# Performance work log

Measured on AMD Instinct MI355X. Metric: run time of the kernel, lower is better.

## Reference

```python
import jax, jax.numpy as jnp
import numpy as np

N = 50000   # nodes
E = 800000  # edges
F = 128     # feat_dim
LN_EPS = 1e-5


def setup_inputs() -> dict:
    key = jax.random.key(0)
    ks = jax.random.split(key, 16)

    def lin(k, fan_in, shape):
        # roughly kaiming-uniform-like scale; exact init is irrelevant for correctness
        return jax.random.normal(k, shape, jnp.float32) * (1.0 / np.sqrt(fan_in))

    inp = {
        "x": jax.random.normal(ks[0], (N, F), jnp.float32),
        "pos": jax.random.normal(ks[1], (N, 3), jnp.float32),
        "edge_index": jax.random.randint(ks[2], (2, E), 0, N, jnp.int64),
        # edge_mlp: Linear(2F+1 -> F), SiLU, Linear(F -> F)
        "ew1": lin(ks[3], 2 * F + 1, (2 * F + 1, F)),
        "eb1": jnp.zeros((F,), jnp.float32),
        "ew2": lin(ks[4], F, (F, F)),
        "eb2": jnp.zeros((F,), jnp.float32),
        # node_mlp: Linear(F -> F), SiLU, Linear(F -> F)
        "nw1": lin(ks[5], F, (F, F)),
        "nb1": jnp.zeros((F,), jnp.float32),
        "nw2": lin(ks[6], F, (F, F)),
        "nb2": jnp.zeros((F,), jnp.float32),
        # coord_mlp: Linear(F -> 1), Tanh
        "cw": lin(ks[7], F, (F, 1)),
        "cb": jnp.zeros((1,), jnp.float32),
        # LayerNorm(F)
        "gamma": jnp.ones((F,), jnp.float32),
        "beta": jnp.zeros((F,), jnp.float32),
    }
    return inp


def reference(x, pos, edge_index, ew1, eb1, ew2, eb2, nw1, nb1, nw2, nb2, cw, cb, gamma, beta):
    row, col = edge_index[0], edge_index[1]

    diff = pos[row] - pos[col]                              # [E, 3]
    dist2 = jnp.sum(diff * diff, axis=1, keepdims=True)     # [E, 1]
    edge_feat = jnp.concatenate([x[row], x[col], dist2], axis=1)  # [E, 2F+1]

    # edge MLP (dropout p=0 -> identity in eval)
    msg = jax.nn.silu(edge_feat @ ew1 + eb1) @ ew2 + eb2    # [E, F]

    # scatter-add messages to source nodes
    agg = jax.ops.segment_sum(msg, row, num_segments=N)     # [N, F]

    # node MLP + residual + LayerNorm
    upd = jax.nn.silu(agg @ nw1 + nb1) @ nw2 + nb2          # [N, F]
    pre = x + upd
    mean = jnp.mean(pre, axis=-1, keepdims=True)
    var = jnp.mean(jnp.square(pre - mean), axis=-1, keepdims=True)
    x_out = gamma * (pre - mean) * jax.lax.rsqrt(var + LN_EPS) + beta

    # coordinate update
    scale = jnp.tanh(msg @ cw + cb)                         # [E, 1]
    delta = jax.ops.segment_sum(scale * diff, row, num_segments=N)  # [N, 3]
    pos_out = pos + delta
    return (x_out, pos_out)
```

## Files before the change

### kernel.cpp

```cpp
#include <hip/hip_runtime.h>
#include <math.h>

#define NN 50000
#define EE 800000
#define FF 128

constexpr float LN_EPS = 1e-5f;
constexpr int NC = (NN + 255) / 256;

typedef float  f32x4  __attribute__((ext_vector_type(4)));
typedef short  s16x8  __attribute__((ext_vector_type(8)));

__device__ __forceinline__ float silu_f(float v) {
    return v / (1.f + __expf(-v));
}

__device__ __forceinline__ unsigned short f2bf(float f) {
    union { float f; unsigned u; } cv; cv.f = f;
    unsigned u = cv.u;
    u += 0x7fffu + ((u >> 16) & 1u);
    return (unsigned short)(u >> 16);
}

__device__ __forceinline__ float bf2f(unsigned short u) {
    union { unsigned u; float f; } cv; cv.u = ((unsigned)u) << 16;
    return cv.f;
}

__global__ __launch_bounds__(256) void convert_x_kernel(
    const float* __restrict__ x, unsigned short* __restrict__ xb)
{
    int i = (blockIdx.x * 256 + threadIdx.x) * 8;
    float4 a = *(const float4*)&x[i];
    float4 b = *(const float4*)&x[i + 4];
    s16x8 o;
    o[0] = (short)f2bf(a.x); o[1] = (short)f2bf(a.y);
    o[2] = (short)f2bf(a.z); o[3] = (short)f2bf(a.w);
    o[4] = (short)f2bf(b.x); o[5] = (short)f2bf(b.y);
    o[6] = (short)f2bf(b.z); o[7] = (short)f2bf(b.w);
    *(s16x8*)&xb[i] = o;
}

__global__ __launch_bounds__(256) void transpose_w_kernel(
    const float* __restrict__ ew1, const float* __restrict__ ew2,
    const float* __restrict__ nw1, const float* __restrict__ nw2,
    unsigned short* __restrict__ ew1T, unsigned short* __restrict__ ew2T,
    unsigned short* __restrict__ nw1T, unsigned short* __restrict__ nw2T)
{
    int o = blockIdx.x * 256 + threadIdx.x;
    if (o < 32768) {
        int n = o >> 8, k = o & 255;
        ew1T[o] = f2bf(ew1[k * FF + n]);
    } else if (o < 49152) {
        int o2 = o - 32768; int n = o2 >> 7, k = o2 & 127;
        ew2T[o2] = f2bf(ew2[k * FF + n]);
    } else if (o < 65536) {
        int o2 = o - 49152; int n = o2 >> 7, k = o2 & 127;
        nw1T[o2] = f2bf(nw1[k * FF + n]);
    } else {
        int o2 = o - 65536; int n = o2 >> 7, k = o2 & 127;
        nw2T[o2] = f2bf(nw2[k * FF + n]);
    }
}

__global__ __launch_bounds__(256) void hist_kernel(
    const int* __restrict__ ei, int* __restrict__ cnt)
{
    int e = blockIdx.x * 256 + threadIdx.x;
    if (e < EE) atomicAdd(&cnt[ei[e]], 1);
}

__global__ __launch_bounds__(256) void chunk_sum_kernel(
    const int* __restrict__ cnt, int* __restrict__ chunkSum)
{
    __shared__ int s[256];
    int t = threadIdx.x;
    int idx = blockIdx.x * 256 + t;
    s[t] = (idx < NN) ? cnt[idx] : 0;
    __syncthreads();
    for (int off = 128; off > 0; off >>= 1) {
        if (t < off) s[t] += s[t + off];
        __syncthreads();
    }
    if (t == 0) chunkSum[blockIdx.x] = s[0];
}

__global__ __launch_bounds__(256) void scan_chunks_kernel(
    const int* __restrict__ chunkSum, int* __restrict__ chunkOff)
{
    __shared__ int s[256];
    int t = threadIdx.x;
    int v = (t < NC) ? chunkSum[t] : 0;
    s[t] = v;
    __syncthreads();
    for (int off = 1; off < 256; off <<= 1) {
        int u = (t >= off) ? s[t - off] : 0;
        __syncthreads();
        s[t] += u;
        __syncthreads();
    }
    if (t < NC) chunkOff[t] = s[t] - v;
}

__global__ __launch_bounds__(256) void scan_kernel(
    const int* __restrict__ cnt, const int* __restrict__ chunkOff,
    int* __restrict__ offs, int* __restrict__ rowStart)
{
    __shared__ int s[256];
    int t = threadIdx.x;
    int idx = blockIdx.x * 256 + t;
    int v = (idx < NN) ? cnt[idx] : 0;
    s[t] = v;
    __syncthreads();
    for (int off = 1; off < 256; off <<= 1) {
        int u = (t >= off) ? s[t - off] : 0;
        __syncthreads();
        s[t] += u;
        __syncthreads();
    }
    if (idx < NN) {
        int st = chunkOff[blockIdx.x] + s[t] - v;
        offs[idx] = st;
        rowStart[idx] = st;
    }
}

__global__ __launch_bounds__(256) void scatter_idx_kernel(
    const int* __restrict__ ei, int* __restrict__ offs,
    int* __restrict__ sRow, int* __restrict__ sCol)
{
    int e = blockIdx.x * 256 + threadIdx.x;
    if (e < EE) {
        int r = ei[e], c = ei[EE + e];
        int p = atomicAdd(&offs[r], 1);
        sRow[p] = r;
        sCol[p] = c;
    }
}

constexpr int EPB   = 64;
constexpr int NTILE = EE / EPB;
constexpr int XAS   = 264;
constexpr int H1S   = 136;

__global__ __launch_bounds__(512, 4) void edgeA_kernel(
    const unsigned short* __restrict__ xb, const float* __restrict__ pos,
    const int* __restrict__ sRow, const int* __restrict__ sCol,
    const unsigned short* __restrict__ ew1T, const float* __restrict__ ew1,
    const float* __restrict__ eb1,
    const unsigned short* __restrict__ ew2T, const float* __restrict__ eb2,
    const float* __restrict__ cw,  const float* __restrict__ cb,
    unsigned short* __restrict__ msgb, float* __restrict__ sSg)
{
    __shared__ float dist2S[EPB];
    __shared__ float sPart[8][EPB];
    __shared__ __align__(16) unsigned short xa  [EPB * XAS];
    __shared__ __align__(16) unsigned short h1  [EPB * H1S];
    __shared__ __align__(16) unsigned short msgL[EPB * H1S];

    const int t   = threadIdx.x;
    const int w   = t >> 6;
    const int l   = t & 63;
    const int l15 = l & 15;
    const int q8  = l >> 4;
    const int n   = w * 16 + l15;

    s16x8 B1[8], B2[4];
    #pragma unroll
    for (int ko = 0; ko < 8; ++ko)
        B1[ko] = *(const s16x8*)(ew1T + (size_t)n * 256 + ko * 32 + q8 * 8);
    #pragma unroll
    for (int ko = 0; ko < 4; ++ko)
        B2[ko] = *(const s16x8*)(ew2T + (size_t)n * 128 + ko * 32 + q8 * 8);
    const float w256 = ew1[256 * FF + n];
    const float b1   = eb1[n];
    const float b2   = eb2[n];
    const float cwc  = cw[n];
    const float cb0  = cb[0];

    const int q   = t & 31;
    const int eB  = t >> 5;
    const int ksel = (q & 15) * 8;
    const int* idxBase = (q < 16) ? sRow : sCol;

    int   nidx[4];
    s16x8 ag[4];
    {
        int e0 = blockIdx.x * EPB;
        #pragma unroll
        for (int i = 0; i < 4; ++i) nidx[i] = idxBase[e0 + eB + 16 * i];
        #pragma unroll
        for (int i = 0; i < 4; ++i) ag[i] = *(const s16x8*)(xb + (size_t)nidx[i] * FF + ksel);
    }

    for (int tile = blockIdx.x; tile < NTILE; tile += gridDim.x) {
        const int e0 = tile * EPB;

        #pragma unroll
        for (int i = 0; i < 4; ++i)
            *(s16x8*)(xa + (eB + 16 * i) * XAS + q * 8) = ag[i];
        if (t < EPB) {
            int r = sRow[e0 + t];
            int c = sCol[e0 + t];
            float dx = pos[r*3+0] - pos[c*3+0];
            float dy = pos[r*3+1] - pos[c*3+1];
            float dz = pos[r*3+2] - pos[c*3+2];
            dist2S[t] = dx*dx + dy*dy + dz*dz;
        }
        __syncthreads();

        {
            int tn  = tile + gridDim.x;
            int e0n = (tn < NTILE) ? tn * EPB : 0;
            #pragma unroll
            for (int i = 0; i < 4; ++i) nidx[i] = idxBase[e0n + eB + 16 * i];
            #pragma unroll
            for (int i = 0; i < 4; ++i) ag[i] = *(const s16x8*)(xb + (size_t)nidx[i] * FF + ksel);
        }

        f32x4 acc[4] = {};
        #pragma unroll
        for (int mt = 0; mt < 4; ++mt) {
            const unsigned short* ar = xa + (mt * 16 + l15) * XAS + q8 * 8;
            #pragma unroll
            for (int ko = 0; ko < 8; ++ko) {
                s16x8 a = *(const s16x8*)(ar + ko * 32);
                acc[mt] = __builtin_amdgcn_mfma_f32_16x16x32_bf16(a, B1[ko], acc[mt], 0, 0, 0);
            }
        }

        #pragma unroll
        for (int mt = 0; mt < 4; ++mt) {
            #pragma unroll
            for (int r = 0; r < 4; ++r) {
                int e = mt * 16 + q8 * 4 + r;
                float v = acc[mt][r] + dist2S[e] * w256 + b1;
                h1[e * H1S + n] = f2bf(silu_f(v));
            }
        }
        __syncthreads();

        f32x4 acc2[4] = {};
        #pragma unroll
        for (int mt = 0; mt < 4; ++mt) {
            const unsigned short* hr = h1 + (mt * 16 + l15) * H1S + q8 * 8;
            #pragma unroll
            for (int ko = 0; ko < 4; ++ko) {
                s16x8 a = *(const s16x8*)(hr + ko * 32);
                acc2[mt] = __builtin_amdgcn_mfma_f32_16x16x32_bf16(a, B2[ko], acc2[mt], 0, 0, 0);
            }
        }

        #pragma unroll
        for (int mt = 0; mt < 4; ++mt) {
            #pragma unroll
            for (int r = 0; r < 4; ++r) {
                float m = acc2[mt][r] + b2;
                float p = m * cwc;
                p += __shfl_xor(p, 1);
                p += __shfl_xor(p, 2);
                p += __shfl_xor(p, 4);
                p += __shfl_xor(p, 8);
                int e = mt * 16 + q8 * 4 + r;
                if (l15 == 0) sPart[w][e] = p;
                msgL[e * H1S + n] = f2bf(m);
            }
        }
        __syncthreads();

        if (t < EPB) {
            float p = 0.f;
            #pragma unroll
            for (int ww = 0; ww < 8; ++ww) p += sPart[ww][t];
            sSg[e0 + t] = tanhf(p + cb0);
        }

        #pragma unroll
        for (int i = 0; i < 2; ++i) {
            int idx = i * 512 + t;
            int e   = idx >> 4;
            int c   = idx & 15;
            *(s16x8*)&msgb[(size_t)(e0 + e) * FF + c * 8] =
                *(const s16x8*)&msgL[e * H1S + c * 8];
        }
    }
}

constexpr int NPB = 16;
constexpr int ABS = 136;

__global__ __launch_bounds__(512) void nodeB_kernel(
    const float* __restrict__ x, const float* __restrict__ pos,
    const unsigned short* __restrict__ msgb, const float* __restrict__ sSg,
    const int* __restrict__ sCol, const int* __restrict__ rowStart,
    const unsigned short* __restrict__ nw1T, const float* __restrict__ nb1,
    const unsigned short* __restrict__ nw2T, const float* __restrict__ nb2,
    const float* __restrict__ gamma, const float* __restrict__ beta,
    float* __restrict__ xout, float* __restrict__ posout)
{
    __shared__ __align__(16) unsigned short aB [NPB * ABS];
    __shared__ __align__(16) unsigned short h1B[NPB * ABS];
    __shared__ float sRedS[8][NPB];
    __shared__ float sRedQ[8][NPB];

    const int t   = threadIdx.x;
    const int w   = t >> 6;
    const int l   = t & 63;
    const int l15 = l & 15;
    const int q8  = l >> 4;
    const int n0  = blockIdx.x * NPB;
    const int n   = w * 16 + l15;

    #pragma unroll
    for (int s = 0; s < 2; ++s) {
        int e  = 2 * w + s;
        int nn = n0 + e;
        int p0 = rowStart[nn];
        int p1 = (nn == NN - 1) ? EE : rowStart[nn + 1];
        float a0=0.f,a1=0.f,a2=0.f,a3=0.f,a4=0.f,a5=0.f,a6=0.f,a7=0.f;
        for (int p = p0 + q8; p < p1; p += 4) {
            s16x8 v = *(const s16x8*)(msgb + (size_t)p * FF + l15 * 8);
            a0 += bf2f((unsigned short)v[0]);
            a1 += bf2f((unsigned short)v[1]);
            a2 += bf2f((unsigned short)v[2]);
            a3 += bf2f((unsigned short)v[3]);
            a4 += bf2f((unsigned short)v[4]);
            a5 += bf2f((unsigned short)v[5]);
            a6 += bf2f((unsigned short)v[6]);
            a7 += bf2f((unsigned short)v[7]);
        }
        a0 += __shfl_xor(a0,16); a1 += __shfl_xor(a1,16);
        a2 += __shfl_xor(a2,16); a3 += __shfl_xor(a3,16);
        a4 += __shfl_xor(a4,16); a5 += __shfl_xor(a5,16);
        a6 += __shfl_xor(a6,16); a7 += __shfl_xor(a7,16);
        a0 += __shfl_xor(a0,32); a1 += __shfl_xor(a1,32);
        a2 += __shfl_xor(a2,32); a3 += __shfl_xor(a3,32);
        a4 += __shfl_xor(a4,32); a5 += __shfl_xor(a5,32);
        a6 += __shfl_xor(a6,32); a7 += __shfl_xor(a7,32);
        if (q8 == 0) {
            s16x8 o;
            o[0]=(short)f2bf(a0); o[1]=(short)f2bf(a1);
            o[2]=(short)f2bf(a2); o[3]=(short)f2bf(a3);
            o[4]=(short)f2bf(a4); o[5]=(short)f2bf(a5);
            o[6]=(short)f2bf(a6); o[7]=(short)f2bf(a7);
            *(s16x8*)(aB + e * ABS + l15 * 8) = o;
        }
    }

    if (t < NPB * 3) {
        int e = t / 3, d = t % 3;
        int nn = n0 + e;
        int p0 = rowStart[nn];
        int p1 = (nn == NN - 1) ? EE : rowStart[nn + 1];
        float pn = pos[nn * 3 + d];
        float sum = 0.f;
        for (int p = p0; p < p1; ++p) {
            int c = sCol[p];
            sum += sSg[p] * (pn - pos[c * 3 + d]);
        }
        posout[nn * 3 + d] = pn + sum;
    }
    __syncthreads();

    f32x4 acc = {};
    {
        const unsigned short* ar = aB + l15 * ABS + q8 * 8;
        #pragma unroll
        for (int ko = 0; ko < 4; ++ko) {
            s16x8 a = *(const s16x8*)(ar + ko * 32);
            s16x8 b = *(const s16x8*)(nw1T + (size_t)n * 128 + ko * 32 + q8 * 8);
            acc = __builtin_amdgcn_mfma_f32_16x16x32_bf16(a, b, acc, 0, 0, 0);
        }
    }
    {
        float bb = nb1[n];
        #pragma unroll
        for (int r = 0; r < 4; ++r) {
            int e = q8 * 4 + r;
            h1B[e * ABS + n] = f2bf(silu_f(acc[r] + bb));
        }
    }
    __syncthreads();

    f32x4 acc2 = {};
    {
        const unsigned short* hr = h1B + l15 * ABS + q8 * 8;
        #pragma unroll
        for (int ko = 0; ko < 4; ++ko) {
            s16x8 a = *(const s16x8*)(hr + ko * 32);
            s16x8 b = *(const s16x8*)(nw2T + (size_t)n * 128 + ko * 32 + q8 * 8);
            acc2 = __builtin_amdgcn_mfma_f32_16x16x32_bf16(a, b, acc2, 0, 0, 0);
        }
    }

    float pre[4];
    {
        float bb = nb2[n];
        #pragma unroll
        for (int r = 0; r < 4; ++r) {
            int e = q8 * 4 + r;
            pre[r] = x[(size_t)(n0 + e) * FF + n] + acc2[r] + bb;
        }
    }
    #pragma unroll
    for (int r = 0; r < 4; ++r) {
        float s = pre[r], sq = pre[r] * pre[r];
        s += __shfl_xor(s, 1);  sq += __shfl_xor(sq, 1);
        s += __shfl_xor(s, 2);  sq += __shfl_xor(sq, 2);
        s += __shfl_xor(s, 4);  sq += __shfl_xor(sq, 4);
        s += __shfl_xor(s, 8);  sq += __shfl_xor(sq, 8);
        if (l15 == 0) {
            int e = q8 * 4 + r;
            sRedS[w][e] = s;
            sRedQ[w][e] = sq;
        }
    }
    __syncthreads();

    {
        float g = gamma[n], bt = beta[n];
        #pragma unroll
        for (int r = 0; r < 4; ++r) {
            int e = q8 * 4 + r;
            float S = 0.f, Q = 0.f;
            #pragma unroll
            for (int ww = 0; ww < 8; ++ww) { S += sRedS[ww][e]; Q += sRedQ[ww][e]; }
            float mean = S * (1.f / FF);
            float var  = Q * (1.f / FF) - mean * mean;
            xout[(size_t)(n0 + e) * FF + n] =
                g * (pre[r] - mean) * rsqrtf(var + LN_EPS) + bt;
        }
    }
}

extern "C" void kernel_launch(void* const* d_in, const int* in_sizes, int n_in,
                              void* d_out, int out_size, void* d_ws, size_t ws_size,
                              hipStream_t stream) {
    const float* x    = (const float*)d_in[0];
    const float* pos  = (const float*)d_in[1];
    const int*   ei   = (const int*)  d_in[2];
    const float* ew1  = (const float*)d_in[3];
    const float* eb1  = (const float*)d_in[4];
    const float* ew2  = (const float*)d_in[5];
    const float* eb2  = (const float*)d_in[6];
    const float* nw1  = (const float*)d_in[7];
    const float* nb1  = (const float*)d_in[8];
    const float* nw2  = (const float*)d_in[9];
    const float* nb2  = (const float*)d_in[10];
    const float* cw   = (const float*)d_in[11];
    const float* cb   = (const float*)d_in[12];
    const float* gam  = (const float*)d_in[13];
    const float* bet  = (const float*)d_in[14];

    float* out    = (float*)d_out;
    float* xout   = out;
    float* posout = out + (size_t)NN * FF;

    auto align256 = [](size_t v) { return (v + 255) & ~(size_t)255; };
    char* ws = (char*)d_ws;

    size_t CNT_B   = align256((size_t)NN * 4);
    size_t OFFS_B  = align256((size_t)NN * 4);
    size_t RST_B   = align256((size_t)NN * 4);
    size_t CHNK_B  = align256((size_t)NC * 4 * 2);
    size_t SROW_B  = align256((size_t)EE * 4);
    size_t XB_B    = align256((size_t)NN * FF * 2);
    size_t EW1T_B  = align256((size_t)128 * 256 * 2);
    size_t WT_B    = align256((size_t)128 * 128 * 2);
    size_t MSGB_B  = align256((size_t)EE * FF * 2);

    size_t o = 0;
    int* cnt       = (int*)(ws + o);  o += CNT_B;
    int* offs      = (int*)(ws + o);  o += OFFS_B;
    int* rowStart  = (int*)(ws + o);  o += RST_B;
    int* chunkSum  = (int*)(ws + o);
    int* chunkOff  = chunkSum + NC;   o += CHNK_B;
    int* sRow      = (int*)(ws + o);  o += SROW_B;
    int* sCol      = (int*)(ws + o);  o += SROW_B;
    unsigned short* xb   = (unsigned short*)(ws + o);  o += XB_B;
    unsigned short* ew1T = (unsigned short*)(ws + o);  o += EW1T_B;
    unsigned short* ew2T = (unsigned short*)(ws + o);  o += WT_B;
    unsigned short* nw1T = (unsigned short*)(ws + o);  o += WT_B;
    unsigned short* nw2T = (unsigned short*)(ws + o);  o += WT_B;
    unsigned short* msgb = (unsigned short*)(ws + o);  o += MSGB_B;
    float*          sSg  = (float*)(ws + o);

    hipMemsetAsync(cnt, 0, CNT_B, stream);

    convert_x_kernel<<<(NN * FF / 8) / 256, 256, 0, stream>>>(x, xb);
    transpose_w_kernel<<<(32768 + 3 * 16384) / 256, 256, 0, stream>>>(
        ew1, ew2, nw1, nw2, ew1T, ew2T, nw1T, nw2T);

    hist_kernel<<<(EE + 255) / 256, 256, 0, stream>>>(ei, cnt);
    chunk_sum_kernel<<<NC, 256, 0, stream>>>(cnt, chunkSum);
    scan_chunks_kernel<<<1, 256, 0, stream>>>(chunkSum, chunkOff);
    scan_kernel<<<NC, 256, 0, stream>>>(cnt, chunkOff, offs, rowStart);
    scatter_idx_kernel<<<(EE + 255) / 256, 256, 0, stream>>>(ei, offs, sRow, sCol);

    edgeA_kernel<<<2048, 512, 0, stream>>>(
        xb, pos, sRow, sCol, ew1T, ew1, eb1, ew2T, eb2, cw, cb, msgb, sSg);

    nodeB_kernel<<<NN / NPB, 512, 0, stream>>>(
        x, pos, msgb, sSg, sCol, rowStart,
        nw1T, nb1, nw2T, nb2, gam, bet, xout, posout);
}
```

Measured before the change: 517.0 us.

## Split node stage into segmented aggregation and batched node-MLP kernels, pack edge indices

Edge row and column indices are packed into one int2 array so each edge needs a single 8-byte load. The old per-node kernel, which gave each node two warps-worth of threads and walked its edges serially for the coordinate delta, is replaced by two kernels. An aggregation kernel streams the contiguous sorted edge range of 64 nodes with run-length accumulation and shared-memory atomics, writing bf16 aggregates and the delta. A node kernel then runs the MLP and LayerNorm on 32 nodes per block. This targets load imbalance and serial loops in the old aggregation, at the cost of an extra launch, an intermediate round trip, and aliasing workspace (aggB reuses xb, delta is stored in posout and read back in place).

After: 572.5 us. 1.11x slower.

```diff
diff --git a/kernel.cpp b/kernel.cpp
--- a/kernel.cpp
+++ b/kernel.cpp
@@ -127,14 +127,13 @@
 
 __global__ __launch_bounds__(256) void scatter_idx_kernel(
     const int* __restrict__ ei, int* __restrict__ offs,
-    int* __restrict__ sRow, int* __restrict__ sCol)
+    int2* __restrict__ sRC)
 {
     int e = blockIdx.x * 256 + threadIdx.x;
     if (e < EE) {
         int r = ei[e], c = ei[EE + e];
         int p = atomicAdd(&offs[r], 1);
-        sRow[p] = r;
-        sCol[p] = c;
+        sRC[p] = make_int2(r, c);
     }
 }
 
@@ -145,7 +144,7 @@
 
 __global__ __launch_bounds__(512, 4) void edgeA_kernel(
     const unsigned short* __restrict__ xb, const float* __restrict__ pos,
-    const int* __restrict__ sRow, const int* __restrict__ sCol,
+    const int2* __restrict__ sRC,
     const unsigned short* __restrict__ ew1T, const float* __restrict__ ew1,
     const float* __restrict__ eb1,
     const unsigned short* __restrict__ ew2T, const float* __restrict__ eb2,
@@ -178,17 +177,20 @@
     const float cwc  = cw[n];
     const float cb0  = cb[0];
 
-    const int q   = t & 31;
-    const int eB  = t >> 5;
+    const int q    = t & 31;
+    const int eB   = t >> 5;
     const int ksel = (q & 15) * 8;
-    const int* idxBase = (q < 16) ? sRow : sCol;
+    const bool useRow = (q < 16);
 
     int   nidx[4];
     s16x8 ag[4];
     {
         int e0 = blockIdx.x * EPB;
         #pragma unroll
-        for (int i = 0; i < 4; ++i) nidx[i] = idxBase[e0 + eB + 16 * i];
+        for (int i = 0; i < 4; ++i) {
+            int2 rc = sRC[e0 + eB + 16 * i];
+            nidx[i] = useRow ? rc.x : rc.y;
+        }
         #pragma unroll
         for (int i = 0; i < 4; ++i) ag[i] = *(const s16x8*)(xb + (size_t)nidx[i] * FF + ksel);
     }
@@ -200,8 +202,8 @@
         for (int i = 0; i < 4; ++i)
             *(s16x8*)(xa + (eB + 16 * i) * XAS + q * 8) = ag[i];
         if (t < EPB) {
-            int r = sRow[e0 + t];
-            int c = sCol[e0 + t];
+            int2 rc = sRC[e0 + t];
+            int r = rc.x, c = rc.y;
             float dx = pos[r*3+0] - pos[c*3+0];
             float dy = pos[r*3+1] - pos[c*3+1];
             float dz = pos[r*3+2] - pos[c*3+2];
@@ -213,7 +215,10 @@
             int tn  = tile + gridDim.x;
             int e0n = (tn < NTILE) ? tn * EPB : 0;
             #pragma unroll
-            for (int i = 0; i < 4; ++i) nidx[i] = idxBase[e0n + eB + 16 * i];
+            for (int i = 0; i < 4; ++i) {
+                int2 rc = sRC[e0n + eB + 16 * i];
+                nidx[i] = useRow ? rc.x : rc.y;
+            }
             #pragma unroll
             for (int i = 0; i < 4; ++i) ag[i] = *(const s16x8*)(xb + (size_t)nidx[i] * FF + ksel);
         }
@@ -286,150 +291,217 @@
     }
 }
 
-constexpr int NPB = 16;
-constexpr int ABS = 136;
-
-__global__ __launch_bounds__(512) void nodeB_kernel(
+constexpr int NB1 = 64;
+constexpr int AST = 132;
+
+__global__ __launch_bounds__(512) void aggB_kernel(
+    const unsigned short* __restrict__ msgb, const float* __restrict__ sSg,
+    const int2* __restrict__ sRC, const int* __restrict__ rowStart,
+    const float* __restrict__ pos,
+    unsigned short* __restrict__ aggB, float* __restrict__ delta)
+{
+    __shared__ float aggL[NB1 * AST];
+    __shared__ float dL[NB1 * 3];
+
+    const int t  = threadIdx.x;
+    const int g  = t >> 4;
+    const int c8 = (t & 15) * 8;
+    const int n0 = blockIdx.x * NB1;
+
+    for (int i = t; i < NB1 * AST; i += 512) aggL[i] = 0.f;
+    if (t < NB1 * 3) dL[t] = 0.f;
+    __syncthreads();
+
+    const int p0 = rowStart[n0];
+    const int p1 = (n0 + NB1 >= NN) ? EE : rowStart[n0 + NB1];
+
+    float acc[8];
+    #pragma unroll
+    for (int j = 0; j < 8; ++j) acc[j] = 0.f;
+    int cur = -1;
+
+    for (int base = p0 + g * 16; base < p1; base += 512) {
+        int rr[16];
+        #pragma unroll
+        for (int i = 0; i < 16; ++i) {
+            int p = base + i;
+            rr[i] = sRC[(p < EE) ? p : (EE - 1)].x;
+        }
+        #pragma unroll
+        for (int i = 0; i < 16; ++i) {
+            int p = base + i;
+            if (p < p1) {
+                int r = rr[i];
+                if (r != cur) {
+                    if (cur >= 0) {
+                        float* dst = aggL + (cur - n0) * AST + c8;
+                        #pragma unroll
+                        for (int j = 0; j < 8; ++j) atomicAdd(dst + j, acc[j]);
+                    }
+                    cur = r;
+                    #pragma unroll
+                    for (int j = 0; j < 8; ++j) acc[j] = 0.f;
+                }
+                s16x8 v = *(const s16x8*)(msgb + (size_t)p * FF + c8);
+                #pragma unroll
+                for (int j = 0; j < 8; ++j) acc[j] += bf2f((unsigned short)v[j]);
+            }
+        }
+    }
+    if (cur >= 0) {
+        float* dst = aggL + (cur - n0) * AST + c8;
+        #pragma unroll
+        for (int j = 0; j < 8; ++j) atomicAdd(dst + j, acc[j]);
+    }
+
+    for (int p = p0 + t; p < p1; p += 512) {
+        int2 rc = sRC[p];
+        float s = sSg[p];
+        int r = rc.x, c = rc.y;
+        float* dd = dL + (r - n0) * 3;
+        atomicAdd(dd + 0, s * (pos[r*3+0] - pos[c*3+0]));
+        atomicAdd(dd + 1, s * (pos[r*3+1] - pos[c*3+1]));
+        atomicAdd(dd + 2, s * (pos[r*3+2] - pos[c*3+2]));
+    }
+    __syncthreads();
+
+    for (int idx = t; idx < NB1 * 16; idx += 512) {
+        int e = idx >> 4, c = (idx & 15) * 8;
+        if (n0 + e < NN) {
+            s16x8 o;
+            #pragma unroll
+            for (int j = 0; j < 8; ++j) o[j] = (short)f2bf(aggL[e * AST + c + j]);
+            *(s16x8*)(aggB + (size_t)(n0 + e) * FF + c) = o;
+        }
+    }
+    if (t < NB1 * 3) {
+        int e = t / 3;
+        if (n0 + e < NN) delta[(size_t)(n0 + e) * 3 + (t % 3)] = dL[t];
+    }
+}
+
+constexpr int NPB2 = 32;
+constexpr int XTS  = 132;
+constexpr int HBS  = 136;
+
+__global__ __launch_bounds__(512) void nodeC_kernel(
     const float* __restrict__ x, const float* __restrict__ pos,
-    const unsigned short* __restrict__ msgb, const float* __restrict__ sSg,
-    const int* __restrict__ sCol, const int* __restrict__ rowStart,
+    const unsigned short* __restrict__ aggB, const float* __restrict__ delta,
     const unsigned short* __restrict__ nw1T, const float* __restrict__ nb1,
     const unsigned short* __restrict__ nw2T, const float* __restrict__ nb2,
     const float* __restrict__ gamma, const float* __restrict__ beta,
     float* __restrict__ xout, float* __restrict__ posout)
 {
-    __shared__ __align__(16) unsigned short aB [NPB * ABS];
-    __shared__ __align__(16) unsigned short h1B[NPB * ABS];
-    __shared__ float sRedS[8][NPB];
-    __shared__ float sRedQ[8][NPB];
+    __shared__ __align__(16) float xT[NPB2 * XTS];
+    __shared__ __align__(16) unsigned short h1B[NPB2 * HBS];
+    __shared__ float sRedS[8][NPB2];
+    __shared__ float sRedQ[8][NPB2];
 
     const int t   = threadIdx.x;
     const int w   = t >> 6;
     const int l   = t & 63;
     const int l15 = l & 15;
     const int q8  = l >> 4;
-    const int n0  = blockIdx.x * NPB;
+    const int n0  = blockIdx.x * NPB2;
     const int n   = w * 16 + l15;
 
     #pragma unroll
-    for (int s = 0; s < 2; ++s) {
-        int e  = 2 * w + s;
-        int nn = n0 + e;
-        int p0 = rowStart[nn];
-        int p1 = (nn == NN - 1) ? EE : rowStart[nn + 1];
-        float a0=0.f,a1=0.f,a2=0.f,a3=0.f,a4=0.f,a5=0.f,a6=0.f,a7=0.f;
-        for (int p = p0 + q8; p < p1; p += 4) {
-            s16x8 v = *(const s16x8*)(msgb + (size_t)p * FF + l15 * 8);
-            a0 += bf2f((unsigned short)v[0]);
-            a1 += bf2f((unsigned short)v[1]);
-            a2 += bf2f((unsigned short)v[2]);
-            a3 += bf2f((unsigned short)v[3]);
-            a4 += bf2f((unsigned short)v[4]);
-            a5 += bf2f((unsigned short)v[5]);
-            a6 += bf2f((unsigned short)v[6]);
-            a7 += bf2f((unsigned short)v[7]);
-        }
-        a0 += __shfl_xor(a0,16); a1 += __shfl_xor(a1,16);
-        a2 += __shfl_xor(a2,16); a3 += __shfl_xor(a3,16);
-        a4 += __shfl_xor(a4,16); a5 += __shfl_xor(a5,16);
-        a6 += __shfl_xor(a6,16); a7 += __shfl_xor(a7,16);
-        a0 += __shfl_xor(a0,32); a1 += __shfl_xor(a1,32);
-        a2 += __shfl_xor(a2,32); a3 += __shfl_xor(a3,32);
-        a4 += __shfl_xor(a4,32); a5 += __shfl_xor(a5,32);
-        a6 += __shfl_xor(a6,32); a7 += __shfl_xor(a7,32);
-        if (q8 == 0) {
-            s16x8 o;
-            o[0]=(short)f2bf(a0); o[1]=(short)f2bf(a1);
-            o[2]=(short)f2bf(a2); o[3]=(short)f2bf(a3);
-            o[4]=(short)f2bf(a4); o[5]=(short)f2bf(a5);
-            o[6]=(short)f2bf(a6); o[7]=(short)f2bf(a7);
-            *(s16x8*)(aB + e * ABS + l15 * 8) = o;
-        }
-    }
-
-    if (t < NPB * 3) {
+    for (int i = 0; i < 2; ++i) {
+        int idx = i * 512 + t;
+        int e = idx >> 5, c = (idx & 31) * 4;
+        int ee = (n0 + e < NN) ? (n0 + e) : (NN - 1);
+        *(float4*)&xT[e * XTS + c] = *(const float4*)&x[(size_t)ee * FF + c];
+    }
+    if (t < NPB2 * 3) {
         int e = t / 3, d = t % 3;
         int nn = n0 + e;
-        int p0 = rowStart[nn];
-        int p1 = (nn == NN - 1) ? EE : rowStart[nn + 1];
-        float pn = pos[nn * 3 + d];
-        float sum = 0.f;
-        for (int p = p0; p < p1; ++p) {
-            int c = sCol[p];
-            sum += sSg[p] * (pn - pos[c * 3 + d]);
-        }
-        posout[nn * 3 + d] = pn + sum;
-    }
-    __syncthreads();
-
-    f32x4 acc = {};
-    {
-        const unsigned short* ar = aB + l15 * ABS + q8 * 8;
+        if (nn < NN)
+            posout[(size_t)nn * 3 + d] = pos[(size_t)nn * 3 + d] + delta[(size_t)nn * 3 + d];
+    }
+
+    f32x4 acc[2] = {};
+    #pragma unroll
+    for (int mt = 0; mt < 2; ++mt) {
+        int row = n0 + mt * 16 + l15;
+        if (row >= NN) row = NN - 1;
+        const unsigned short* ar = aggB + (size_t)row * FF + q8 * 8;
         #pragma unroll
         for (int ko = 0; ko < 4; ++ko) {
             s16x8 a = *(const s16x8*)(ar + ko * 32);
             s16x8 b = *(const s16x8*)(nw1T + (size_t)n * 128 + ko * 32 + q8 * 8);
-            acc = __builtin_amdgcn_mfma_f32_16x16x32_bf16(a, b, acc, 0, 0, 0);
+            acc[mt] = __builtin_amdgcn_mfma_f32_16x16x32_bf16(a, b, acc[mt], 0, 0, 0);
         }
     }
     {
         float bb = nb1[n];
         #pragma unroll
-        for (int r = 0; r < 4; ++r) {
-            int e = q8 * 4 + r;
-            h1B[e * ABS + n] = f2bf(silu_f(acc[r] + bb));
-        }
-    }
-    __syncthreads();
-
-    f32x4 acc2 = {};
-    {
-        const unsigned short* hr = h1B + l15 * ABS + q8 * 8;
+        for (int mt = 0; mt < 2; ++mt)
+            #pragma unroll
+            for (int r = 0; r < 4; ++r) {
+                int e = mt * 16 + q8 * 4 + r;
+                h1B[e * HBS + n] = f2bf(silu_f(acc[mt][r] + bb));
+            }
+    }
+    __syncthreads();
+
+    f32x4 acc2[2] = {};
+    #pragma unroll
+    for (int mt = 0; mt < 2; ++mt) {
+        const unsigned short* hr = h1B + (mt * 16 + l15) * HBS + q8 * 8;
         #pragma unroll
         for (int ko = 0; ko < 4; ++ko) {
             s16x8 a = *(const s16x8*)(hr + ko * 32);
             s16x8 b = *(const s16x8*)(nw2T + (size_t)n * 128 + ko * 32 + q8 * 8);
-            acc2 = __builtin_amdgcn_mfma_f32_16x16x32_bf16(a, b, acc2, 0, 0, 0);
-        }
-    }
-
-    float pre[4];
+            acc2[mt] = __builtin_amdgcn_mfma_f32_16x16x32_bf16(a, b, acc2[mt], 0, 0, 0);
+        }
+    }
+
+    float pre[2][4];
     {
         float bb = nb2[n];
         #pragma unroll
+        for (int mt = 0; mt < 2; ++mt)
+            #pragma unroll
+            for (int r = 0; r < 4; ++r) {
+                int e = mt * 16 + q8 * 4 + r;
+                pre[mt][r] = xT[e * XTS + n] + acc2[mt][r] + bb;
+            }
+    }
+    #pragma unroll
+    for (int mt = 0; mt < 2; ++mt)
+        #pragma unroll
         for (int r = 0; r < 4; ++r) {
-            int e = q8 * 4 + r;
-            pre[r] = x[(size_t)(n0 + e) * FF + n] + acc2[r] + bb;
-        }
-    }
-    #pragma unroll
-    for (int r = 0; r < 4; ++r) {
-        float s = pre[r], sq = pre[r] * pre[r];
-        s += __shfl_xor(s, 1);  sq += __shfl_xor(sq, 1);
-        s += __shfl_xor(s, 2);  sq += __shfl_xor(sq, 2);
-        s += __shfl_xor(s, 4);  sq += __shfl_xor(sq, 4);
-        s += __shfl_xor(s, 8);  sq += __shfl_xor(sq, 8);
-        if (l15 == 0) {
-            int e = q8 * 4 + r;
-            sRedS[w][e] = s;
-            sRedQ[w][e] = sq;
-        }
-    }
+            float s = pre[mt][r], sq = pre[mt][r] * pre[mt][r];
+            s += __shfl_xor(s, 1);  sq += __shfl_xor(sq, 1);
+            s += __shfl_xor(s, 2);  sq += __shfl_xor(sq, 2);
+            s += __shfl_xor(s, 4);  sq += __shfl_xor(sq, 4);
+            s += __shfl_xor(s, 8);  sq += __shfl_xor(sq, 8);
+            if (l15 == 0) {
+                int e = mt * 16 + q8 * 4 + r;
+                sRedS[w][e] = s;
+                sRedQ[w][e] = sq;
+            }
+        }
     __syncthreads();
 
     {
         float g = gamma[n], bt = beta[n];
         #pragma unroll
-        for (int r = 0; r < 4; ++r) {
-            int e = q8 * 4 + r;
-            float S = 0.f, Q = 0.f;
-            #pragma unroll
-            for (int ww = 0; ww < 8; ++ww) { S += sRedS[ww][e]; Q += sRedQ[ww][e]; }
-            float mean = S * (1.f / FF);
-            float var  = Q * (1.f / FF) - mean * mean;
-            xout[(size_t)(n0 + e) * FF + n] =
-                g * (pre[r] - mean) * rsqrtf(var + LN_EPS) + bt;
-        }
+        for (int mt = 0; mt < 2; ++mt)
+            #pragma unroll
+            for (int r = 0; r < 4; ++r) {
+                int e = mt * 16 + q8 * 4 + r;
+                int nn = n0 + e;
+                if (nn < NN) {
+                    float S = 0.f, Q = 0.f;
+                    #pragma unroll
+                    for (int ww = 0; ww < 8; ++ww) { S += sRedS[ww][e]; Q += sRedQ[ww][e]; }
+                    float mean = S * (1.f / FF);
+                    float var  = Q * (1.f / FF) - mean * mean;
+                    xout[(size_t)nn * FF + n] =
+                        g * (pre[mt][r] - mean) * rsqrtf(var + LN_EPS) + bt;
+                }
+            }
     }
 }
 
@@ -463,7 +535,7 @@
     size_t OFFS_B  = align256((size_t)NN * 4);
     size_t RST_B   = align256((size_t)NN * 4);
     size_t CHNK_B  = align256((size_t)NC * 4 * 2);
-    size_t SROW_B  = align256((size_t)EE * 4);
+    size_t SRC_B   = align256((size_t)EE * 8);
     size_t XB_B    = align256((size_t)NN * FF * 2);
     size_t EW1T_B  = align256((size_t)128 * 256 * 2);
     size_t WT_B    = align256((size_t)128 * 128 * 2);
@@ -475,8 +547,7 @@
     int* rowStart  = (int*)(ws + o);  o += RST_B;
     int* chunkSum  = (int*)(ws + o);
     int* chunkOff  = chunkSum + NC;   o += CHNK_B;
-    int* sRow      = (int*)(ws + o);  o += SROW_B;
-    int* sCol      = (int*)(ws + o);  o += SROW_B;
+    int2* sRC      = (int2*)(ws + o); o += SRC_B;
     unsigned short* xb   = (unsigned short*)(ws + o);  o += XB_B;
     unsigned short* ew1T = (unsigned short*)(ws + o);  o += EW1T_B;
     unsigned short* ew2T = (unsigned short*)(ws + o);  o += WT_B;
@@ -485,6 +556,9 @@
     unsigned short* msgb = (unsigned short*)(ws + o);  o += MSGB_B;
     float*          sSg  = (float*)(ws + o);
 
+    unsigned short* aggB  = xb;
+    float*          delta = posout;
+
     hipMemsetAsync(cnt, 0, CNT_B, stream);
 
     convert_x_kernel<<<(NN * FF / 8) / 256, 256, 0, stream>>>(x, xb);
@@ -495,12 +569,14 @@
     chunk_sum_kernel<<<NC, 256, 0, stream>>>(cnt, chunkSum);
     scan_chunks_kernel<<<1, 256, 0, stream>>>(chunkSum, chunkOff);
     scan_kernel<<<NC, 256, 0, stream>>>(cnt, chunkOff, offs, rowStart);
-    scatter_idx_kernel<<<(EE + 255) / 256, 256, 0, stream>>>(ei, offs, sRow, sCol);
+    scatter_idx_kernel<<<(EE + 255) / 256, 256, 0, stream>>>(ei, offs, sRC);
 
     edgeA_kernel<<<2048, 512, 0, stream>>>(
-        xb, pos, sRow, sCol, ew1T, ew1, eb1, ew2T, eb2, cw, cb, msgb, sSg);
-
-    nodeB_kernel<<<NN / NPB, 512, 0, stream>>>(
-        x, pos, msgb, sSg, sCol, rowStart,
-        nw1T, nb1, nw2T, nb2, gam, bet, xout, posout);
-}
+        xb, pos, sRC, ew1T, ew1, eb1, ew2T, eb2, cw, cb, msgb, sSg);
+
+    aggB_kernel<<<(NN + NB1 - 1) / NB1, 512, 0, stream>>>(
+        msgb, sSg, sRC, rowStart, pos, aggB, delta);
+
+    nodeC_kernel<<<(NN + NPB2 - 1) / NPB2, 512, 0, stream>>>(
+        x, pos, aggB, delta, nw1T, nb1, nw2T, nb2, gam, bet, xout, posout);
+}
```
